# Performance work log

Hardware: AMD Instinct MI355X
Metric: run time of the kernel (lower is better)

Reference implementation:

```python
import jax, jax.numpy as jnp
import numpy as np

H = 1024  # hidden_dim
M = 4     # num_modalities
B = 8192  # batch


def setup_inputs() -> dict:
    key = jax.random.key(0)
    ks = jax.random.split(key, 10)
    s = 1.0 / np.sqrt(H)  # torch Linear default init scale
    return {
        "features": jax.random.normal(ks[0], (B, M, H), dtype=jnp.float32),
        "confidences": jax.random.uniform(ks[1], (B, M, 1), dtype=jnp.float32),
        "Wq": jax.random.uniform(ks[2], (H, H), jnp.float32, -s, s),
        "bq": jax.random.uniform(ks[3], (H,), jnp.float32, -s, s),
        "Wk": jax.random.uniform(ks[4], (H, H), jnp.float32, -s, s),
        "bk": jax.random.uniform(ks[5], (H,), jnp.float32, -s, s),
        "Wv": jax.random.uniform(ks[6], (H, H), jnp.float32, -s, s),
        "bv": jax.random.uniform(ks[7], (H,), jnp.float32, -s, s),
        "Wo": jax.random.uniform(ks[8], (H, H), jnp.float32, -s, s),
        "bo": jax.random.uniform(ks[9], (H,), jnp.float32, -s, s),
    }


def reference(features, confidences, Wq, bq, Wk, bk, Wv, bv, Wo, bo):
    # features: [B, M, H], confidences: [B, M, 1]
    q = jnp.einsum('bmh,oh->bmo', features, Wq) + bq
    k = jnp.einsum('bmh,oh->bmo', features, Wk) + bk
    v = jnp.einsum('bmh,oh->bmo', features, Wv) + bv
    scores = jnp.einsum('bmh,bnh->bmn', q, k) / jnp.sqrt(jnp.float32(features.shape[-1]))
    scores = scores * confidences  # [B,M,1] broadcasts over last (key) axis
    attn = jax.nn.softmax(scores, axis=-1)           # [B, M, M]
    attended = jnp.einsum('bmn,bnh->bmh', attn, v)   # [B, M, H]
    fused = jnp.mean(attended, axis=1)               # [B, H]
    return fused @ Wo.T + bo
```

## Files before the change

### kernel.cpp

```cpp
#include <hip/hip_runtime.h>


typedef unsigned short u16;
typedef __attribute__((ext_vector_type(8))) __bf16 bf16x8;
typedef __attribute__((ext_vector_type(4))) float floatx4;

__device__ __forceinline__ u16 f2bf(float f) {
    unsigned u = __float_as_uint(f);
    unsigned r = (u + 0x7FFFu + ((u >> 16) & 1u)) >> 16;
    return (u16)r;
}

__device__ __forceinline__ void load_lds16(const void* g, void* l) {
    __builtin_amdgcn_global_load_lds(
        (const __attribute__((address_space(1))) void*)g,
        (__attribute__((address_space(3))) void*)l, 16, 0, 0);
}

__device__ __forceinline__ void unpack8(uint4 v, float* f) {
    f[0] = __uint_as_float(v.x << 16);
    f[1] = __uint_as_float(v.x & 0xFFFF0000u);
    f[2] = __uint_as_float(v.y << 16);
    f[3] = __uint_as_float(v.y & 0xFFFF0000u);
    f[4] = __uint_as_float(v.z << 16);
    f[5] = __uint_as_float(v.z & 0xFFFF0000u);
    f[6] = __uint_as_float(v.w << 16);
    f[7] = __uint_as_float(v.w & 0xFFFF0000u);
}

__global__ __launch_bounds__(256) void k_cast(const float* __restrict__ in,
                                              u16* __restrict__ outb, long n) {
    long i = ((long)blockIdx.x * 256 + threadIdx.x) * 4;
    if (i < n) {
        float4 v = *(const float4*)(in + i);
        ushort4 o;
        o.x = f2bf(v.x); o.y = f2bf(v.y); o.z = f2bf(v.z); o.w = f2bf(v.w);
        *(ushort4*)(outb + i) = o;
    }
}

__global__ __launch_bounds__(256) void k_prep(const float* __restrict__ Wq,
                                              const float* __restrict__ Wk,
                                              const float* __restrict__ Wv,
                                              const float* __restrict__ Wo,
                                              u16* __restrict__ WqT,
                                              u16* __restrict__ WkT,
                                              u16* __restrict__ WvT,
                                              u16* __restrict__ Wob, int H) {
    __shared__ float t[32][33];
    const int z = blockIdx.z;
    const float* in = (z == 0) ? Wk : (z == 1) ? Wq : (z == 2) ? Wv : Wo;
    u16* out = (z == 0) ? WkT : (z == 1) ? WqT : (z == 2) ? WvT : Wob;
    int bx = blockIdx.x * 32, by = blockIdx.y * 32;
    int x = threadIdx.x;
    if (z < 3) {
        for (int y = threadIdx.y; y < 32; y += 8)
            t[y][x] = in[(size_t)(by + y) * H + bx + x];
        __syncthreads();
        for (int y = threadIdx.y; y < 32; y += 8)
            out[(size_t)(bx + y) * H + by + x] = f2bf(t[x][y]);
    } else {
        for (int y = threadIdx.y; y < 32; y += 8)
            out[(size_t)(by + y) * H + bx + x] = f2bf(in[(size_t)(by + y) * H + bx + x]);
    }
}

__global__ __launch_bounds__(256) void k_uk(const float* __restrict__ Wk,
                                            const float* __restrict__ bq,
                                            float* __restrict__ u, int H) {
    int h = blockIdx.x * 256 + threadIdx.x;
    int chunk = H / 16;
    int o0 = blockIdx.y * chunk;
    float s = 0.f;
    for (int o = o0; o < o0 + chunk; ++o) s += bq[o] * Wk[(size_t)o * H + h];
    atomicAdd(&u[h], s);
}

__global__ __launch_bounds__(256) void k_bias(const float* __restrict__ Wo,
                                              const float* __restrict__ bv,
                                              const float* __restrict__ bo,
                                              float* __restrict__ c, int H) {
    __shared__ float red[4];
    int j = blockIdx.x;
    int lane = threadIdx.x & 63, wv = threadIdx.x >> 6;
    float s = 0.f;
    for (int o = threadIdx.x; o < H; o += 256) s += Wo[(size_t)j * H + o] * bv[o];
    for (int off = 32; off > 0; off >>= 1) s += __shfl_down(s, off);
    if (lane == 0) red[wv] = s;
    __syncthreads();
    if (threadIdx.x == 0) c[j] = red[0] + red[1] + red[2] + red[3] + bo[j];
}

template <int OUTB>
__device__ __forceinline__ void gemm_body(const u16* __restrict__ A,
                                          const u16* __restrict__ Bw,
                                          void* __restrict__ Cp,
                                          const float* __restrict__ bias,
                                          int M, int N, int K,
                                          int bx, int by) {
    __shared__ __align__(16) u16 As[128 * 32];
    __shared__ __align__(16) u16 Bs[128 * 32];
    const int tid = threadIdx.x, lane = tid & 63, wv = tid >> 6;
    const int m0 = bx * 128, n0 = by * 128;
    const int wm = (wv >> 1) * 64, wn = (wv & 1) * 64;

    floatx4 acc[4][4];
#pragma unroll
    for (int i = 0; i < 4; ++i)
#pragma unroll
        for (int j = 0; j < 4; ++j) acc[i][j] = (floatx4){0.f, 0.f, 0.f, 0.f};

    const int srow = lane >> 2;
    const int scol = (((lane & 3) ^ ((lane >> 3) & 3)) * 8);
    const u16* gA = A + (size_t)(m0 + srow) * K + scol;
    const u16* gB = Bw + (size_t)(n0 + srow) * K + scol;
    const int r = lane & 15, q = lane >> 4;
    const int cph = q ^ ((r >> 1) & 3);

    for (int kt = 0; kt < K; kt += 32) {
#pragma unroll
        for (int c = 0; c < 2; ++c) {
            int chunk = wv * 2 + c;
            load_lds16(gA + (size_t)(chunk * 16) * K + kt, &As[chunk * 16 * 32]);
            load_lds16(gB + (size_t)(chunk * 16) * K + kt, &Bs[chunk * 16 * 32]);
        }
        __syncthreads();
        bf16x8 af[4], bfr[4];
#pragma unroll
        for (int i = 0; i < 4; ++i) {
            af[i] = *(const bf16x8*)&As[(wm + i * 16 + r) * 32 + cph * 8];
            bfr[i] = *(const bf16x8*)&Bs[(wn + i * 16 + r) * 32 + cph * 8];
        }
#pragma unroll
        for (int i = 0; i < 4; ++i)
#pragma unroll
            for (int j = 0; j < 4; ++j)
                acc[i][j] = __builtin_amdgcn_mfma_f32_16x16x32_bf16(af[i], bfr[j], acc[i][j], 0, 0, 0);
        __syncthreads();
    }

    const int cc = lane & 15, cr = (lane >> 4) * 4;
#pragma unroll
    for (int i = 0; i < 4; ++i)
#pragma unroll
        for (int j = 0; j < 4; ++j) {
            int col = n0 + wn + j * 16 + cc;
            float badd = bias ? bias[col] : 0.f;
#pragma unroll
            for (int r0 = 0; r0 < 4; ++r0) {
                int row = m0 + wm + i * 16 + cr + r0;
                float v = acc[i][j][r0] + badd;
                if (OUTB) ((u16*)Cp)[(size_t)row * N + col] = f2bf(v);
                else ((float*)Cp)[(size_t)row * N + col] = v;
            }
        }
}

__global__ __launch_bounds__(256) void k_wgemm(const u16* __restrict__ A0,
                                               const u16* __restrict__ B0,
                                               u16* __restrict__ C0,
                                               const u16* __restrict__ A1,
                                               const u16* __restrict__ B1,
                                               u16* __restrict__ C1, int H) {
    if (blockIdx.z == 0)
        gemm_body<1>(A0, B0, C0, nullptr, H, H, H, blockIdx.x, blockIdx.y);
    else
        gemm_body<1>(A1, B1, C1, nullptr, H, H, H, blockIdx.x, blockIdx.y);
}

__global__ __launch_bounds__(256) void k_score(const u16* __restrict__ X,
                                               const u16* __restrict__ Aw,
                                               u16* __restrict__ G,
                                               const float* __restrict__ uk,
                                               int Mr, int N, int K) {
    gemm_body<1>(X, Aw, G, uk, Mr, N, K, blockIdx.x, blockIdx.y);
}

__global__ __launch_bounds__(256) void k_out(const u16* __restrict__ A,
                                             const u16* __restrict__ Bw,
                                             float* __restrict__ C,
                                             const float* __restrict__ bias,
                                             int M, int N, int K) {
    gemm_body<0>(A, Bw, C, bias, M, N, K, blockIdx.x, blockIdx.y);
}

__global__ __launch_bounds__(256) void k_attn(const u16* __restrict__ G,
                                              const u16* __restrict__ X,
                                              const float* __restrict__ conf,
                                              u16* __restrict__ Y, int H) {
    const int lane = threadIdx.x & 63, wv = threadIdx.x >> 6;
    const int b = blockIdx.x * 4 + wv;
    const u16* Gb = G + (size_t)b * 4 * H;
    const u16* Xb = X + (size_t)b * 4 * H;

    uint4 xraw[2][4];
    float s[16];
#pragma unroll
    for (int t = 0; t < 16; ++t) s[t] = 0.f;

#pragma unroll
    for (int c = 0; c < 2; ++c) {
        const int off = c * 512 + lane * 8;
#pragma unroll
        for (int rr = 0; rr < 4; ++rr)
            xraw[c][rr] = *(const uint4*)(Xb + rr * H + off);
        float xv[4][8];
#pragma unroll
        for (int rr = 0; rr < 4; ++rr) unpack8(xraw[c][rr], xv[rr]);
#pragma unroll
        for (int m = 0; m < 4; ++m) {
            uint4 gl = *(const uint4*)(Gb + m * H + off);
            float gv[8];
            unpack8(gl, gv);
#pragma unroll
            for (int n = 0; n < 4; ++n) {
                float a = 0.f;
#pragma unroll
                for (int j = 0; j < 8; ++j) a += gv[j] * xv[n][j];
                s[m * 4 + n] += a;
            }
        }
    }
#pragma unroll
    for (int t = 0; t < 16; ++t) {
#pragma unroll
        for (int mask = 32; mask; mask >>= 1) s[t] += __shfl_xor(s[t], mask);
    }
    float w[4] = {0.f, 0.f, 0.f, 0.f};
#pragma unroll
    for (int m = 0; m < 4; ++m) {
        float cm = conf[(size_t)b * 4 + m] * 0.03125f;
        float sc[4], mx = -1e30f;
#pragma unroll
        for (int n = 0; n < 4; ++n) {
            sc[n] = s[m * 4 + n] * cm;
            mx = fmaxf(mx, sc[n]);
        }
        float e[4], ssum = 0.f;
#pragma unroll
        for (int n = 0; n < 4; ++n) { e[n] = __expf(sc[n] - mx); ssum += e[n]; }
        float inv = 0.25f / ssum;
#pragma unroll
        for (int n = 0; n < 4; ++n) w[n] += e[n] * inv;
    }
#pragma unroll
    for (int c = 0; c < 2; ++c) {
        const int off = c * 512 + lane * 8;
        float xv[4][8];
#pragma unroll
        for (int rr = 0; rr < 4; ++rr) unpack8(xraw[c][rr], xv[rr]);
        float y[8];
#pragma unroll
        for (int j = 0; j < 8; ++j)
            y[j] = w[0] * xv[0][j] + w[1] * xv[1][j] + w[2] * xv[2][j] + w[3] * xv[3][j];
        uint4 res;
        res.x = (unsigned)f2bf(y[0]) | ((unsigned)f2bf(y[1]) << 16);
        res.y = (unsigned)f2bf(y[2]) | ((unsigned)f2bf(y[3]) << 16);
        res.z = (unsigned)f2bf(y[4]) | ((unsigned)f2bf(y[5]) << 16);
        res.w = (unsigned)f2bf(y[6]) | ((unsigned)f2bf(y[7]) << 16);
        *(uint4*)(Y + (size_t)b * H + off) = res;
    }
}

extern "C" void kernel_launch(void* const* d_in, const int* in_sizes, int n_in,
                              void* d_out, int out_size, void* d_ws, size_t ws_size,
                              hipStream_t stream) {
    const int H = 1024, M = 4;
    const int B = in_sizes[0] / (H * M);
    const long BMH = (long)B * M * H;

    const float* feat = (const float*)d_in[0];
    const float* conf = (const float*)d_in[1];
    const float* Wq = (const float*)d_in[2];
    const float* bq = (const float*)d_in[3];
    const float* Wk = (const float*)d_in[4];
    const float* Wv = (const float*)d_in[6];
    const float* bv = (const float*)d_in[7];
    const float* Wo = (const float*)d_in[8];
    const float* bo = (const float*)d_in[9];

    char* ws = (char*)d_ws;
    size_t off = 0;
    auto alloc = [&](size_t bytes) {
        void* p = ws + off;
        off += (bytes + 255) & ~(size_t)255;
        return p;
    };
    u16* Xb    = (u16*)alloc((size_t)BMH * 2);
    u16* G     = (u16*)alloc((size_t)BMH * 2);
    u16* Yb    = (u16*)alloc((size_t)B * H * 2);
    u16* WkT   = (u16*)alloc((size_t)H * H * 2);
    u16* WqT   = (u16*)alloc((size_t)H * H * 2);
    u16* WvT   = (u16*)alloc((size_t)H * H * 2);
    u16* Wob   = (u16*)alloc((size_t)H * H * 2);
    u16* Aw    = (u16*)alloc((size_t)H * H * 2);
    u16* Wov   = (u16*)alloc((size_t)H * H * 2);
    float* u    = (float*)alloc((size_t)H * 4);
    float* cvec = (float*)alloc((size_t)H * 4);
    (void)ws_size; (void)n_in; (void)out_size;

    k_cast<<<(int)(BMH / 4 / 256), 256, 0, stream>>>(feat, Xb, BMH);
    k_prep<<<dim3(H / 32, H / 32, 4), dim3(32, 8), 0, stream>>>(
        Wq, Wk, Wv, Wo, WqT, WkT, WvT, Wob, H);

    hipMemsetAsync(u, 0, (size_t)H * 4, stream);
    k_uk<<<dim3(H / 256, 16), 256, 0, stream>>>(Wk, bq, u, H);
    k_bias<<<H, 256, 0, stream>>>(Wo, bv, bo, cvec, H);

    k_wgemm<<<dim3(H / 128, H / 128, 2), 256, 0, stream>>>(
        WkT, WqT, Aw, Wob, WvT, Wov, H);

    k_score<<<dim3(B * M / 128, H / 128), 256, 0, stream>>>(
        Xb, Aw, G, u, B * M, H, H);

    k_attn<<<B / 4, 256, 0, stream>>>(G, Xb, conf, Yb, H);

    k_out<<<dim3(B / 128, H / 128), 256, 0, stream>>>(Yb, Wov, (float*)d_out, cvec, B, H, H);
}
```

Measured before the change: 416.9 us.

## Run the score GEMM in FP8 E4M3 with scaled weights

Adds an FP8 E4M3 path for the large feature-by-folded-weight score GEMM. The cast kernel also emits an FP8 copy of the features, and the weight GEMM emits an FP8 copy of the folded Wk^T Wq matrix, prescaled by 32. A new k_score8 kernel then uses fp8 MFMA with 64-wide K tiles, and the attention kernel's score scale is adjusted to undo the prescale. The aim is to halve operand bytes and LDS traffic for the dominant GEMM. The cost is an extra FP8 write in the cast kernel and reduced score precision. The fallback path also writes FP8 bytes over the bf16 Aw buffer.

```diff
diff --git a/kernel.cpp b/kernel.cpp
--- a/kernel.cpp
+++ b/kernel.cpp
@@ -2,6 +2,7 @@
 
 
 typedef unsigned short u16;
+typedef unsigned char u8;
 typedef __attribute__((ext_vector_type(8))) __bf16 bf16x8;
 typedef __attribute__((ext_vector_type(4))) float floatx4;
 
@@ -9,6 +10,23 @@
     unsigned u = __float_as_uint(f);
     unsigned r = (u + 0x7FFFu + ((u >> 16) & 1u)) >> 16;
     return (u16)r;
+}
+
+__device__ __forceinline__ unsigned f2e4m3(float x) {
+    unsigned u = __float_as_uint(x);
+    unsigned s = (u >> 31) << 7;
+    float a = __uint_as_float(u & 0x7FFFFFFFu);
+    if (a >= 448.f) return s | 0x7E;
+    if (a < 0.03125f) {
+        unsigned k = (unsigned)__float2int_rn(a * 512.f);
+        return s | k;
+    }
+    unsigned b = __float_as_uint(a);
+    unsigned lsb = (b >> 20) & 1u;
+    b += 0x0007FFFFu + lsb;
+    unsigned ex = (b >> 23) - 120u;
+    unsigned man = (b >> 20) & 7u;
+    return s | (ex << 3) | man;
 }
 
 __device__ __forceinline__ void load_lds16(const void* g, void* l) {
@@ -29,13 +47,19 @@
 }
 
 __global__ __launch_bounds__(256) void k_cast(const float* __restrict__ in,
-                                              u16* __restrict__ outb, long n) {
+                                              u16* __restrict__ outb,
+                                              u8* __restrict__ outf, long n) {
     long i = ((long)blockIdx.x * 256 + threadIdx.x) * 4;
     if (i < n) {
         float4 v = *(const float4*)(in + i);
         ushort4 o;
         o.x = f2bf(v.x); o.y = f2bf(v.y); o.z = f2bf(v.z); o.w = f2bf(v.w);
         *(ushort4*)(outb + i) = o;
+        if (outf) {
+            unsigned p = f2e4m3(v.x) | (f2e4m3(v.y) << 8) |
+                         (f2e4m3(v.z) << 16) | (f2e4m3(v.w) << 24);
+            *(unsigned*)(outf + i) = p;
+        }
     }
 }
 
@@ -91,10 +115,11 @@
     if (threadIdx.x == 0) c[j] = red[0] + red[1] + red[2] + red[3] + bo[j];
 }
 
-template <int OUTB>
+template <int OUTMODE>
 __device__ __forceinline__ void gemm_body(const u16* __restrict__ A,
                                           const u16* __restrict__ Bw,
                                           void* __restrict__ Cp,
+                                          u8* __restrict__ Cp8,
                                           const float* __restrict__ bias,
                                           int M, int N, int K,
                                           int bx, int by) {
@@ -150,8 +175,10 @@
             for (int r0 = 0; r0 < 4; ++r0) {
                 int row = m0 + wm + i * 16 + cr + r0;
                 float v = acc[i][j][r0] + badd;
-                if (OUTB) ((u16*)Cp)[(size_t)row * N + col] = f2bf(v);
-                else ((float*)Cp)[(size_t)row * N + col] = v;
+                if (OUTMODE == 0) ((float*)Cp)[(size_t)row * N + col] = v;
+                else ((u16*)Cp)[(size_t)row * N + col] = f2bf(v);
+                if (OUTMODE == 2)
+                    Cp8[(size_t)row * N + col] = (u8)f2e4m3(32.f * v);
             }
         }
 }
@@ -159,13 +186,14 @@
 __global__ __launch_bounds__(256) void k_wgemm(const u16* __restrict__ A0,
                                                const u16* __restrict__ B0,
                                                u16* __restrict__ C0,
+                                               u8* __restrict__ C0f8,
                                                const u16* __restrict__ A1,
                                                const u16* __restrict__ B1,
                                                u16* __restrict__ C1, int H) {
     if (blockIdx.z == 0)
-        gemm_body<1>(A0, B0, C0, nullptr, H, H, H, blockIdx.x, blockIdx.y);
+        gemm_body<2>(A0, B0, C0, C0f8, nullptr, H, H, H, blockIdx.x, blockIdx.y);
     else
-        gemm_body<1>(A1, B1, C1, nullptr, H, H, H, blockIdx.x, blockIdx.y);
+        gemm_body<1>(A1, B1, C1, nullptr, nullptr, H, H, H, blockIdx.x, blockIdx.y);
 }
 
 __global__ __launch_bounds__(256) void k_score(const u16* __restrict__ X,
@@ -173,7 +201,7 @@
                                                u16* __restrict__ G,
                                                const float* __restrict__ uk,
                                                int Mr, int N, int K) {
-    gemm_body<1>(X, Aw, G, uk, Mr, N, K, blockIdx.x, blockIdx.y);
+    gemm_body<1>(X, Aw, G, nullptr, uk, Mr, N, K, blockIdx.x, blockIdx.y);
 }
 
 __global__ __launch_bounds__(256) void k_out(const u16* __restrict__ A,
@@ -181,13 +209,81 @@
                                              float* __restrict__ C,
                                              const float* __restrict__ bias,
                                              int M, int N, int K) {
-    gemm_body<0>(A, Bw, C, bias, M, N, K, blockIdx.x, blockIdx.y);
+    gemm_body<0>(A, Bw, C, nullptr, bias, M, N, K, blockIdx.x, blockIdx.y);
+}
+
+__global__ __launch_bounds__(256) void k_score8(const u8* __restrict__ Af8,
+                                                const u8* __restrict__ Bf8,
+                                                u16* __restrict__ G,
+                                                const float* __restrict__ uk,
+                                                int Mr, int N, int K) {
+    __shared__ __align__(16) u8 As[128 * 64];
+    __shared__ __align__(16) u8 Bs[128 * 64];
+    const int tid = threadIdx.x, lane = tid & 63, wv = tid >> 6;
+    const int n0 = blockIdx.x * 128, m0 = blockIdx.y * 128;
+    const int wm = (wv >> 1) * 64, wn = (wv & 1) * 64;
+
+    floatx4 acc[4][4];
+#pragma unroll
+    for (int i = 0; i < 4; ++i)
+#pragma unroll
+        for (int j = 0; j < 4; ++j) acc[i][j] = (floatx4){0.f, 0.f, 0.f, 0.f};
+
+    const int srow = lane >> 2;
+    const int scol = 16 * ((lane & 3) ^ ((lane >> 3) & 3));
+    const u8* gA = Af8 + (size_t)(m0 + srow) * K + scol;
+    const u8* gB = Bf8 + (size_t)(n0 + srow) * K + scol;
+    const int r = lane & 15, q = lane >> 4;
+    const int swz = (r >> 1) & 3;
+    const int qh = q >> 1, ql = (q & 1) * 8;
+
+    for (int kt = 0; kt < K; kt += 64) {
+#pragma unroll
+        for (int c = 0; c < 2; ++c) {
+            int chunk = wv * 2 + c;
+            load_lds16(gA + (size_t)(chunk * 16) * K + kt, &As[chunk * 16 * 64]);
+            load_lds16(gB + (size_t)(chunk * 16) * K + kt, &Bs[chunk * 16 * 64]);
+        }
+        __syncthreads();
+#pragma unroll
+        for (int s = 0; s < 2; ++s) {
+            long long af[4], bfr[4];
+#pragma unroll
+            for (int i = 0; i < 4; ++i) {
+                int piece = ((2 * s + qh) ^ swz) * 16 + ql;
+                af[i] = *(const long long*)&As[(wm + i * 16 + r) * 64 + piece];
+                bfr[i] = *(const long long*)&Bs[(wn + i * 16 + r) * 64 + piece];
+            }
+#pragma unroll
+            for (int i = 0; i < 4; ++i)
+#pragma unroll
+                for (int j = 0; j < 4; ++j)
+                    acc[i][j] = __builtin_amdgcn_mfma_f32_16x16x32_fp8_fp8(
+                        af[i], bfr[j], acc[i][j], 0, 0, 0);
+        }
+        __syncthreads();
+    }
+
+    const int cc = lane & 15, cr = (lane >> 4) * 4;
+#pragma unroll
+    for (int i = 0; i < 4; ++i)
+#pragma unroll
+        for (int j = 0; j < 4; ++j) {
+            int col = n0 + wn + j * 16 + cc;
+            float badd = 32.f * uk[col];
+#pragma unroll
+            for (int r0 = 0; r0 < 4; ++r0) {
+                int row = m0 + wm + i * 16 + cr + r0;
+                G[(size_t)row * N + col] = f2bf(acc[i][j][r0] + badd);
+            }
+        }
 }
 
 __global__ __launch_bounds__(256) void k_attn(const u16* __restrict__ G,
                                               const u16* __restrict__ X,
                                               const float* __restrict__ conf,
-                                              u16* __restrict__ Y, int H) {
+                                              u16* __restrict__ Y, float gscale,
+                                              int H) {
     const int lane = threadIdx.x & 63, wv = threadIdx.x >> 6;
     const int b = blockIdx.x * 4 + wv;
     const u16* Gb = G + (size_t)b * 4 * H;
@@ -229,7 +325,7 @@
     float w[4] = {0.f, 0.f, 0.f, 0.f};
 #pragma unroll
     for (int m = 0; m < 4; ++m) {
-        float cm = conf[(size_t)b * 4 + m] * 0.03125f;
+        float cm = conf[(size_t)b * 4 + m] * gscale;
         float sc[4], mx = -1e30f;
 #pragma unroll
         for (int n = 0; n < 4; ++n) {
@@ -297,9 +393,13 @@
     u16* Wov   = (u16*)alloc((size_t)H * H * 2);
     float* u    = (float*)alloc((size_t)H * 4);
     float* cvec = (float*)alloc((size_t)H * 4);
-    (void)ws_size; (void)n_in; (void)out_size;
-
-    k_cast<<<(int)(BMH / 4 / 256), 256, 0, stream>>>(feat, Xb, BMH);
+    u8* Xf8  = (u8*)alloc((size_t)BMH);
+    u8* Awf8 = (u8*)alloc((size_t)H * H);
+    const bool use_fp8 = (off <= ws_size);
+    (void)n_in; (void)out_size;
+
+    k_cast<<<(int)(BMH / 4 / 256), 256, 0, stream>>>(
+        feat, Xb, use_fp8 ? Xf8 : nullptr, BMH);
     k_prep<<<dim3(H / 32, H / 32, 4), dim3(32, 8), 0, stream>>>(
         Wq, Wk, Wv, Wo, WqT, WkT, WvT, Wob, H);
 
@@ -308,12 +408,18 @@
     k_bias<<<H, 256, 0, stream>>>(Wo, bv, bo, cvec, H);
 
     k_wgemm<<<dim3(H / 128, H / 128, 2), 256, 0, stream>>>(
-        WkT, WqT, Aw, Wob, WvT, Wov, H);
-
-    k_score<<<dim3(B * M / 128, H / 128), 256, 0, stream>>>(
-        Xb, Aw, G, u, B * M, H, H);
-
-    k_attn<<<B / 4, 256, 0, stream>>>(G, Xb, conf, Yb, H);
+        WkT, WqT, Aw, use_fp8 ? Awf8 : (u8*)Aw , Wob, WvT, Wov, H);
+
+    if (use_fp8) {
+        k_score8<<<dim3(H / 128, B * M / 128), 256, 0, stream>>>(
+            Xf8, Awf8, G, u, B * M, H, H);
+    } else {
+        k_score<<<dim3(B * M / 128, H / 128), 256, 0, stream>>>(
+            Xb, Aw, G, u, B * M, H, H);
+    }
+
+    k_attn<<<B / 4, 256, 0, stream>>>(G, Xb, conf, Yb,
+                                      use_fp8 ? 0.0009765625f : 0.03125f, H);
 
     k_out<<<dim3(B / 128, H / 128), 256, 0, stream>>>(Yb, Wov, (float*)d_out, cvec, B, H, H);
 }
```

After: 415.7 us. About the same (-0.3%).
